# Kernel optimization log

Hardware: AMD Instinct MI355X
Metric: run time of the kernel (lower is better)

The kernel has to match this reference:

```python
import jax, jax.numpy as jnp
import numpy as np

B, N, D, H, I = 16, 1024, 1024, 16, 4096
HS = D // H  # 64
EPS = 1e-5


def setup_inputs() -> dict:
    key = jax.random.key(0)
    ks = jax.random.split(key, 8)
    w = lambda k, shape: (jax.random.normal(k, shape, jnp.float32) * 0.02)
    return {
        'hidden_states': jax.random.normal(ks[0], (B, N, D), jnp.float32),
        'ln1_g': jnp.ones((D,), jnp.float32), 'ln1_b': jnp.zeros((D,), jnp.float32),
        'ln2_g': jnp.ones((D,), jnp.float32), 'ln2_b': jnp.zeros((D,), jnp.float32),
        'wq': w(ks[1], (D, D)), 'bq': jnp.zeros((D,), jnp.float32),
        'wk': w(ks[2], (D, D)), 'bk': jnp.zeros((D,), jnp.float32),
        'wv': w(ks[3], (D, D)), 'bv': jnp.zeros((D,), jnp.float32),
        'w1': w(ks[4], (D, I)), 'b1': jnp.zeros((I,), jnp.float32),
        'w2': w(ks[5], (I, D)), 'b2': jnp.zeros((D,), jnp.float32),
    }


def _layernorm(x, g, b):
    m = jnp.mean(x, axis=-1, keepdims=True)
    v = jnp.var(x, axis=-1, keepdims=True)
    return (x - m) * jax.lax.rsqrt(v + EPS) * g + b


def _split_heads(t):
    # Faithful to transpose_for_scores: reshape (B,N,HS,H) -> (B,H,N,HS)
    # i.e. head h takes the strided feature slice t[..., h::H].
    b, n, _ = t.shape
    return t.reshape(b, n, HS, H).transpose(0, 3, 1, 2)


def _vit_layer(x, ln1_g, ln1_b, ln2_g, ln2_b, wq, bq, wk, bk, wv, bv, w1, b1, w2, b2):
    h = _layernorm(x, ln1_g, ln1_b)
    q = _split_heads(h @ wq + bq)  # [B,H,N,HS]
    k = _split_heads(h @ wk + bk)
    v = _split_heads(h @ wv + bv)
    scores = jax.nn.softmax(jnp.einsum('bhqd,bhkd->bhqk', q, k) / np.sqrt(HS).astype(np.float32), axis=-1)
    attn = jnp.einsum('bhqk,bhkd->bhqd', scores, v)          # [B,H,N,HS]
    attn = attn.transpose(0, 2, 1, 3).reshape(x.shape)       # head-major merge (as in source)
    x = x + attn
    h = _layernorm(x, ln2_g, ln2_b)
    mlp = jax.nn.silu(h @ w1 + b1) @ w2 + b2
    return x + mlp


def reference(hidden_states, ln1_g, ln1_b, ln2_g, ln2_b, wq, bq, wk, bk, wv, bv, w1, b1, w2, b2):
    return _vit_layer(hidden_states, ln1_g, ln1_b, ln2_g, ln2_b, wq, bq, wk, bk, wv, bv, w1, b1, w2, b2)
```

## Files before the change

### kernel.cpp

```cpp
#include <hip/hip_runtime.h>
#include <hip/hip_bf16.h>
#include <stdint.h>

typedef __bf16 bf16;
typedef bf16 bf16x8 __attribute__((ext_vector_type(8)));
typedef bf16 bf16x4 __attribute__((ext_vector_type(4)));
typedef float f32x4 __attribute__((ext_vector_type(4)));

static __device__ __forceinline__ f32x4 mfma16(bf16x8 a, bf16x8 b, f32x4 c) {
    return __builtin_amdgcn_mfma_f32_16x16x32_bf16(a, b, c, 0, 0, 0);
}

static __device__ __forceinline__ void gld16(const bf16* g, bf16* l) {
    __builtin_amdgcn_global_load_lds((const __attribute__((address_space(1))) void*)g,
                                     (__attribute__((address_space(3))) void*)l, 16, 0, 0);
}

static __device__ __forceinline__ uint32_t pkbf(float a, float b) {
    union { bf16 h[2]; uint32_t u; } u_;
    u_.h[0] = (bf16)a; u_.h[1] = (bf16)b;
    return u_.u;
}

static __device__ __forceinline__ void xcd_supertile(int gdx, int gdy,
                                                     int& bx, int& by) {
    const int orig = blockIdx.y * gdx + blockIdx.x;
    const int xcd = orig & 7;
    const int idx = orig >> 3;
    const int CBY = gdy >> 3;
    const int gx = (gdx >= 4) ? 4 : gdx;
    const int gy = (CBY >= 4) ? 4 : CBY;
    const int cells = gx * gy;
    const int st = idx / cells, off = idx % cells;
    const int nstx = gdx / gx;
    const int stx = st % nstx, sty = st / nstx;
    bx = stx * gx + off % gx;
    by = xcd * CBY + sty * gy + off / gx;
}

static __device__ __forceinline__ void tcast_body_p1(
    const float* __restrict__ src, bf16* __restrict__ dst,
    int R, int C, int bx, int by, int tid, float (*t)[33]) {
    const int tx = tid & 31, ty = tid >> 5;
    const int c0 = bx * 32, r0 = by * 32;
#pragma unroll
    for (int j = 0; j < 4; ++j)
        t[ty + j * 8][tx] = src[(size_t)(r0 + ty + j * 8) * C + c0 + tx];
    __syncthreads();
#pragma unroll
    for (int j = 0; j < 4; ++j) {
        const int c = c0 + ty + j * 8;
        const int cp = ((c & 15) << 6) | (c >> 4);
        dst[(size_t)cp * R + r0 + tx] = (bf16)t[tx][ty + j * 8];
    }
}

static __device__ __forceinline__ void tcast_body_p0(
    const float* __restrict__ src, bf16* __restrict__ dst,
    int R, int C, int bx, int by, int tid, float (*t)[33]) {
    const int tx = tid & 31, ty = tid >> 5;
    const int c0 = bx * 32, r0 = by * 32;
#pragma unroll
    for (int j = 0; j < 4; ++j)
        t[ty + j * 8][tx] = src[(size_t)(r0 + ty + j * 8) * C + c0 + tx];
    __syncthreads();
#pragma unroll
    for (int j = 0; j < 4; ++j) {
        const int c = c0 + ty + j * 8;
        dst[(size_t)c * R + r0 + tx] = (bf16)t[tx][ty + j * 8];
    }
}

__global__ __launch_bounds__(256)
void prologue_kernel(const float* __restrict__ wq, const float* __restrict__ wk,
                     const float* __restrict__ wv, const float* __restrict__ w1,
                     const float* __restrict__ w2,
                     const float* __restrict__ bq, const float* __restrict__ bk,
                     const float* __restrict__ bv,
                     const float* __restrict__ x, const float* __restrict__ gg,
                     const float* __restrict__ bb,
                     bf16* __restrict__ Wqkvt, bf16* __restrict__ W1t,
                     bf16* __restrict__ W2t, float* __restrict__ bqkvp,
                     bf16* __restrict__ Xln) {
    __shared__ float t[32][33];
    __shared__ float red[8];
    const int blk = blockIdx.x, tid = threadIdx.x;

    if (blk < 3072) {
        const int seg = blk >> 10, b = blk & 1023;
        const float* src = (seg == 0) ? wq : (seg == 1) ? wk : wv;
        tcast_body_p1(src, Wqkvt + (size_t)seg * 1024 * 1024,
                      1024, 1024, b & 31, b >> 5, tid, t);
    } else if (blk < 7168) {
        const int b = blk - 3072;
        tcast_body_p0(w1, W1t, 1024, 4096, b & 127, b >> 7, tid, t);
    } else if (blk < 11264) {
        const int b = blk - 7168;
        tcast_body_p0(w2, W2t, 4096, 1024, b & 31, b >> 5, tid, t);
    } else if (blk < 11276) {
        const int i = (blk - 11264) * 256 + tid;
        const int seg = i >> 10, c = i & 1023;
        const int src = ((c & 63) << 4) | (c >> 6);
        const float* b = (seg == 0) ? bq : (seg == 1) ? bk : bv;
        bqkvp[i] = b[src];
    } else {
        const int row = blk - 11276;
        const int lane = tid & 63, wid = tid >> 6;
        const float4 v = ((const float4*)(x + (size_t)row * 1024))[tid];
        float s  = v.x + v.y + v.z + v.w;
        float s2 = v.x * v.x + v.y * v.y + v.z * v.z + v.w * v.w;
#pragma unroll
        for (int m = 1; m <= 32; m <<= 1) {
            s  += __shfl_xor(s,  m);
            s2 += __shfl_xor(s2, m);
        }
        if (lane == 0) { red[wid] = s; red[wid + 4] = s2; }
        __syncthreads();
        float ts  = red[0] + red[1] + red[2] + red[3];
        float ts2 = red[4] + red[5] + red[6] + red[7];
        float mean = ts * (1.f / 1024.f);
        float var  = ts2 * (1.f / 1024.f) - mean * mean;
        float rs   = rsqrtf(var + 1e-5f);
        const float4 gv = ((const float4*)gg)[tid];
        const float4 bv4 = ((const float4*)bb)[tid];
        bf16x4 o;
        o[0] = (bf16)((v.x - mean) * rs * gv.x + bv4.x);
        o[1] = (bf16)((v.y - mean) * rs * gv.y + bv4.y);
        o[2] = (bf16)((v.z - mean) * rs * gv.z + bv4.z);
        o[3] = (bf16)((v.w - mean) * rs * gv.w + bv4.w);
        *(bf16x4*)(Xln + (size_t)row * 1024 + tid * 4) = o;
    }
}

__global__ __launch_bounds__(256)
void ln_kernel(const float* __restrict__ x, const float* __restrict__ gg,
               const float* __restrict__ bb, bf16* __restrict__ out) {
    __shared__ float red[8];
    const int row = blockIdx.x, tid = threadIdx.x;
    const int lane = tid & 63, wid = tid >> 6;
    const float4 v = ((const float4*)(x + (size_t)row * 1024))[tid];
    float s  = v.x + v.y + v.z + v.w;
    float s2 = v.x * v.x + v.y * v.y + v.z * v.z + v.w * v.w;
#pragma unroll
    for (int m = 1; m <= 32; m <<= 1) {
        s  += __shfl_xor(s,  m);
        s2 += __shfl_xor(s2, m);
    }
    if (lane == 0) { red[wid] = s; red[wid + 4] = s2; }
    __syncthreads();
    float ts  = red[0] + red[1] + red[2] + red[3];
    float ts2 = red[4] + red[5] + red[6] + red[7];
    float mean = ts * (1.f / 1024.f);
    float var  = ts2 * (1.f / 1024.f) - mean * mean;
    float rs   = rsqrtf(var + 1e-5f);
    const float4 gv = ((const float4*)gg)[tid];
    const float4 bv = ((const float4*)bb)[tid];
    bf16x4 o;
    o[0] = (bf16)((v.x - mean) * rs * gv.x + bv.x);
    o[1] = (bf16)((v.y - mean) * rs * gv.y + bv.y);
    o[2] = (bf16)((v.z - mean) * rs * gv.z + bv.z);
    o[3] = (bf16)((v.w - mean) * rs * gv.w + bv.w);
    *(bf16x4*)(out + (size_t)row * 1024 + tid * 4) = o;
}

template <int MODE>
__global__ __launch_bounds__(256)
void gemm_bt(const bf16* __restrict__ A, const bf16* __restrict__ Bt,
             int M, int N, int K,
             const float* __restrict__ bias_a,
             const float* __restrict__ resid, float* __restrict__ outF,
             bf16* __restrict__ oQ, bf16* __restrict__ oK, bf16* __restrict__ oV,
             bf16* __restrict__ oB) {
    __shared__ alignas(16) bf16 As[3][128 * 32];
    __shared__ alignas(16) bf16 Bs[3][128 * 32];
    const int tid = threadIdx.x;
    const int wid = tid >> 6, lane = tid & 63;
    const int li = lane & 15, g = lane >> 4;

    int bx, by;
    xcd_supertile(gridDim.x, gridDim.y, bx, by);
    const int row0 = by * 128, col0 = bx * 128;

    const int gsrc = ((tid & 3) ^ ((tid >> 3) & 3)) * 8;
    const bf16* gA0 = A + (size_t)(row0 + (tid >> 2)) * K + gsrc;
    const bf16* gA1 = A + (size_t)(row0 + 64 + (tid >> 2)) * K + gsrc;
    const bf16* gB0 = Bt + (size_t)(col0 + (tid >> 2)) * K + gsrc;
    const bf16* gB1 = Bt + (size_t)(col0 + 64 + (tid >> 2)) * K + gsrc;

    const int wr = wid >> 1, wc = wid & 1;
    f32x4 acc[4][4] = {};

    const int nt = K >> 5;
#pragma unroll
    for (int p = 0; p < 2; ++p) {
        const int kk = p << 5;
        gld16(gA0 + kk, &As[p][wid * 512]);
        gld16(gA1 + kk, &As[p][wid * 512 + 2048]);
        gld16(gB0 + kk, &Bs[p][wid * 512]);
        gld16(gB1 + kk, &Bs[p][wid * 512 + 2048]);
    }

    const int sa = (li >> 1) & 3;
    const int rdoff = (g ^ sa) * 8;

    int cur = 0;
    for (int t = 0; t < nt; ++t) {
        if (t + 2 < nt) {
            const int k2 = (t + 2) << 5;
            const int nb = (cur + 2) % 3;
            gld16(gA0 + k2, &As[nb][wid * 512]);
            gld16(gA1 + k2, &As[nb][wid * 512 + 2048]);
            gld16(gB0 + k2, &Bs[nb][wid * 512]);
            gld16(gB1 + k2, &Bs[nb][wid * 512 + 2048]);
            asm volatile("s_waitcnt vmcnt(8)" ::: "memory");
        } else if (t + 1 < nt) {
            asm volatile("s_waitcnt vmcnt(4)" ::: "memory");
        } else {
            asm volatile("s_waitcnt vmcnt(0)" ::: "memory");
        }
        __builtin_amdgcn_s_barrier();
        __builtin_amdgcn_sched_barrier(0);

        bf16x8 af[4], bg[4];
        const bf16* pa = &As[cur][(wr * 64 + li) * 32 + rdoff];
        const bf16* pb = &Bs[cur][(wc * 64 + li) * 32 + rdoff];
#pragma unroll
        for (int i = 0; i < 4; ++i) af[i] = *(const bf16x8*)(pa + i * 512);
#pragma unroll
        for (int j = 0; j < 4; ++j) bg[j] = *(const bf16x8*)(pb + j * 512);
#pragma unroll
        for (int i = 0; i < 4; ++i)
#pragma unroll
            for (int j = 0; j < 4; ++j)
                acc[i][j] = mfma16(af[i], bg[j], acc[i][j]);
        __builtin_amdgcn_sched_barrier(0);
        __builtin_amdgcn_s_barrier();
        cur = (cur + 1) % 3;
    }

    if (MODE == 0) {
        const int seg = col0 >> 10;
        const int h   = ((col0 & 1023) >> 6) + wc;
        const int bb  = row0 >> 10;
        const int n0  = (row0 & 1023) + wr * 64;
        float bias[4];
#pragma unroll
        for (int j = 0; j < 4; ++j) bias[j] = bias_a[col0 + wc * 64 + j * 16 + li];

        if (seg == 2) {
#pragma unroll
            for (int i = 0; i < 4; ++i)
#pragma unroll
                for (int j = 0; j < 4; ++j) {
                    const int d = j * 16 + li;
                    bf16x4 pv;
#pragma unroll
                    for (int r = 0; r < 4; ++r) pv[r] = (bf16)(acc[i][j][r] + bias[j]);
                    *(bf16x4*)(oV + ((size_t)(bb * 16 + h) * 64 + d) * 1024
                                   + n0 + i * 16 + g * 4) = pv;
                }
        } else {
            char* ep = (wid < 3) ? ((char*)&As[0][0] + wid * 8192)
                                 : ((char*)&Bs[0][0]);
            const float scale = (seg == 0) ? 0.125f : 1.0f;
            bf16* og = (seg == 0) ? oQ : oK;
#pragma unroll
            for (int i = 0; i < 4; ++i)
#pragma unroll
                for (int j = 0; j < 4; ++j)
#pragma unroll
                    for (int r = 0; r < 4; ++r) {
                        const int rr = i * 16 + g * 4 + r;
                        const int byte = (rr * 128 + (j * 16 + li) * 2) ^ ((rr & 7) << 4);
                        *(bf16*)(ep + byte) = (bf16)((acc[i][j][r] + bias[j]) * scale);
                    }
            bf16* gb = og + ((size_t)(bb * 16 + h) * 1024 + n0) * 64;
#pragma unroll
            for (int t = 0; t < 8; ++t) {
                const int rr = t * 8 + (lane >> 3);
                const int d0 = (lane & 7) * 8;
                const int byte = (rr * 128 + d0 * 2) ^ ((rr & 7) << 4);
                bf16x8 val = *(const bf16x8*)(ep + byte);
                *(bf16x8*)(gb + (size_t)rr * 64 + d0) = val;
            }
        }
    } else {
#pragma unroll
        for (int i = 0; i < 4; ++i) {
            const int row = row0 + wr * 64 + i * 16 + g * 4;
#pragma unroll
            for (int j = 0; j < 4; ++j) {
                const int col = col0 + wc * 64 + j * 16 + li;
                f32x4 v = acc[i][j];
                if (MODE == 1) {
                    const float bias = bias_a[col];
#pragma unroll
                    for (int r = 0; r < 4; ++r) {
                        float val = v[r] + bias;
                        val = val / (1.f + __expf(-val));
                        oB[(size_t)(row + r) * N + col] = (bf16)val;
                    }
                } else {
                    const float bias = bias_a[col];
#pragma unroll
                    for (int r = 0; r < 4; ++r) {
                        const size_t idx = (size_t)(row + r) * N + col;
                        outF[idx] = v[r] + bias + resid[idx];
                    }
                }
            }
        }
    }
}

template <int MODE>
__global__ __launch_bounds__(512, 2)
void gemm256(const bf16* __restrict__ A, const bf16* __restrict__ Bt,
             int M, int N, int K,
             const float* __restrict__ bias_a,
             const float* __restrict__ resid, float* __restrict__ outF,
             bf16* __restrict__ oB) {
    __shared__ alignas(16) bf16 As[2][256 * 64];
    __shared__ alignas(16) bf16 Bs[2][256 * 64];
    const int tid = threadIdx.x;
    const int wid = tid >> 6, lane = tid & 63;
    const int li = lane & 15, g = lane >> 4;
    const int wm = wid >> 2, wn = wid & 3;

    int bx, by;
    xcd_supertile(gridDim.x, gridDim.y, bx, by);
    const int row0 = by * 256, col0 = bx * 256;

    const int gsrc = ((tid & 7) ^ ((tid >> 3) & 7)) << 3;
    const bf16* gA = A + (size_t)(row0 + (tid >> 3)) * K + gsrc;
    const bf16* gB = Bt + (size_t)(col0 + (tid >> 3)) * K + gsrc;

    f32x4 acc[8][4] = {};
    const int nt = K >> 6;

    const int ro0 = (((0 * 4 + g) ^ (li & 7)) << 3);
    const int ro1 = (((1 * 4 + g) ^ (li & 7)) << 3);

#pragma unroll
    for (int j = 0; j < 4; ++j) {
        gld16(gA + (size_t)(64 * j) * K, &As[0][j * 4096 + (wid << 9)]);
        gld16(gB + (size_t)(64 * j) * K, &Bs[0][j * 4096 + (wid << 9)]);
    }

#define RDA(dst, p)                                                        \
    do {                                                                   \
        _Pragma("unroll")                                                  \
        for (int ii = 0; ii < 2; ++ii) {                                   \
            const int rr = wm * 128 + ((p) * 2 + ii) * 16 + li;            \
            dst[ii][0] = *(const bf16x8*)(At + rr * 64 + ro0);             \
            dst[ii][1] = *(const bf16x8*)(At + rr * 64 + ro1);             \
        }                                                                  \
    } while (0)

#define MFMAP(p, src)                                                      \
    do {                                                                   \
        __builtin_amdgcn_s_setprio(1);                                     \
        _Pragma("unroll")                                                  \
        for (int ii = 0; ii < 2; ++ii)                                     \
            _Pragma("unroll")                                              \
            for (int jf = 0; jf < 4; ++jf) {                               \
                acc[(p) * 2 + ii][jf] = mfma16(src[ii][0], bfr[jf][0],     \
                                               acc[(p) * 2 + ii][jf]);     \
                acc[(p) * 2 + ii][jf] = mfma16(src[ii][1], bfr[jf][1],     \
                                               acc[(p) * 2 + ii][jf]);     \
            }                                                              \
        __builtin_amdgcn_s_setprio(0);                                     \
    } while (0)

    for (int t = 0; t < nt; ++t) {
        asm volatile("s_waitcnt vmcnt(0)" ::: "memory");
        __builtin_amdgcn_s_barrier();
        __builtin_amdgcn_sched_barrier(0);

        const bf16* At = &As[t & 1][0];
        const bf16* Bl = &Bs[t & 1][0];
        bf16* Asn = &As[(t & 1) ^ 1][0];
        bf16* Bsn = &Bs[(t & 1) ^ 1][0];
        const bool pf = (t + 1 < nt);
        const size_t koff = (size_t)(t + 1) << 6;

        bf16x8 bfr[4][2];
#pragma unroll
        for (int jf = 0; jf < 4; ++jf) {
            const int rb = wn * 64 + jf * 16 + li;
            bfr[jf][0] = *(const bf16x8*)(Bl + rb * 64 + ro0);
            bfr[jf][1] = *(const bf16x8*)(Bl + rb * 64 + ro1);
        }
        bf16x8 afA[2][2], afB[2][2];
        RDA(afA, 0);
        if (pf) {
            gld16(gB + koff,                   Bsn + (wid << 9));
            gld16(gB + (size_t)64 * K + koff,  Bsn + 4096 + (wid << 9));
            gld16(gB + (size_t)128 * K + koff, Bsn + 2 * 4096 + (wid << 9));
            gld16(gB + (size_t)192 * K + koff, Bsn + 3 * 4096 + (wid << 9));
        }
        RDA(afB, 1);
        asm volatile("s_waitcnt lgkmcnt(4)" ::: "memory");
        __builtin_amdgcn_sched_barrier(0);
        MFMAP(0, afA);

        RDA(afA, 2);
        asm volatile("s_waitcnt lgkmcnt(4)" ::: "memory");
        __builtin_amdgcn_sched_barrier(0);
        MFMAP(1, afB);

        if (pf) {
            gld16(gA + koff,                   Asn + (wid << 9));
            gld16(gA + (size_t)64 * K + koff,  Asn + 4096 + (wid << 9));
            gld16(gA + (size_t)128 * K + koff, Asn + 2 * 4096 + (wid << 9));
            gld16(gA + (size_t)192 * K + koff, Asn + 3 * 4096 + (wid << 9));
        }
        RDA(afB, 3);
        asm volatile("s_waitcnt lgkmcnt(4)" ::: "memory");
        __builtin_amdgcn_sched_barrier(0);
        MFMAP(2, afA);

        asm volatile("s_waitcnt lgkmcnt(0)" ::: "memory");
        __builtin_amdgcn_sched_barrier(0);
        MFMAP(3, afB);
    }
#undef RDA
#undef MFMAP

#pragma unroll
    for (int i = 0; i < 8; ++i) {
        const int row = row0 + wm * 128 + i * 16 + g * 4;
#pragma unroll
        for (int jf = 0; jf < 4; ++jf) {
            const int col = col0 + wn * 64 + jf * 16 + li;
            const float bias = bias_a[col];
            if (MODE == 1) {
#pragma unroll
                for (int r = 0; r < 4; ++r) {
                    float val = acc[i][jf][r] + bias;
                    val = val / (1.f + __expf(-val));
                    oB[(size_t)(row + r) * N + col] = (bf16)val;
                }
            } else {
#pragma unroll
                for (int r = 0; r < 4; ++r) {
                    const size_t idx = (size_t)(row + r) * N + col;
                    outF[idx] = acc[i][jf][r] + bias + resid[idx];
                }
            }
        }
    }
}

__global__ __launch_bounds__(256)
void attn_kernel(const bf16* __restrict__ Q, const bf16* __restrict__ Kb,
                 const bf16* __restrict__ Vt, const float* __restrict__ x,
                 float* __restrict__ out) {
    __shared__ alignas(16) bf16 Kl[2][4096];
    __shared__ alignas(16) bf16 Vl[2][4096];
    __shared__ alignas(16) char Ps[4][4096];
    const int tid = threadIdx.x, wid = tid >> 6, lane = tid & 63;
    const int li = lane & 15, g = lane >> 4;
    const int bid = blockIdx.x;
    const int bh = (bid & 7) + ((bid >> 6) << 3);
    const int qt = (bid >> 3) & 7;
    const int b = bh >> 4, h = bh & 15;
    const size_t base = (size_t)bh << 16;
    const bf16* Qp = Q + base + (size_t)(qt * 128 + wid * 32) * 64;
    const bf16* Kp = Kb + base;
    const bf16* Vp = Vt + base;
    char* psw = Ps[wid];
    const int swz = (li & 7) << 4;

    const int srow = lane >> 3;
    const int sslot = (lane & 7) ^ srow;

    bf16x8 aq[2][2];
#pragma unroll
    for (int fr = 0; fr < 2; ++fr)
#pragma unroll
        for (int ks = 0; ks < 2; ++ks)
            aq[fr][ks] = *(const bf16x8*)(Qp + (fr * 16 + li) * 64 + ks * 32 + g * 8);

#pragma unroll
    for (int hh = 0; hh < 2; ++hh) {
        const int r = wid * 16 + hh * 8 + srow;
        gld16(Kp + (size_t)r * 64 + sslot * 8, &Kl[0][(wid * 16 + hh * 8) * 64]);
        gld16(Vp + (size_t)r * 1024 + sslot * 8, &Vl[0][(wid * 16 + hh * 8) * 64]);
    }
    asm volatile("s_waitcnt vmcnt(0)" ::: "memory");
    __builtin_amdgcn_s_barrier();

    f32x4 o[2][4] = {};
    float mrun[2] = {-1e30f, -1e30f}, lrun[2] = {0.f, 0.f};

    for (int kt = 0; kt < 16; ++kt) {
        const int cur = kt & 1;
        const bf16* Kt = Kl[cur];
        const bf16* Vtl = Vl[cur];
        if (kt < 15) {
            const int nb = (kt + 1) * 64;
#pragma unroll
            for (int hh = 0; hh < 2; ++hh) {
                const int r = wid * 16 + hh * 8 + srow;
                gld16(Kp + (size_t)(nb + r) * 64 + sslot * 8,
                      &Kl[cur ^ 1][(wid * 16 + hh * 8) * 64]);
                gld16(Vp + (size_t)r * 1024 + nb + sslot * 8,
                      &Vl[cur ^ 1][(wid * 16 + hh * 8) * 64]);
            }
            asm volatile("s_waitcnt vmcnt(4)" ::: "memory");
        } else {
            asm volatile("s_waitcnt vmcnt(0)" ::: "memory");
        }
        __builtin_amdgcn_s_barrier();
        __builtin_amdgcn_sched_barrier(0);

        f32x4 s[2][4] = {};
        __builtin_amdgcn_s_setprio(1);
#pragma unroll
        for (int jc = 0; jc < 4; ++jc) {
            const int row = jc * 16 + li;
#pragma unroll
            for (int ks = 0; ks < 2; ++ks) {
                bf16x8 kf = *(const bf16x8*)(Kt + row * 64 + (((ks * 4 + g) ^ (li & 7)) * 8));
                s[0][jc] = mfma16(kf, aq[0][ks], s[0][jc]);
                s[1][jc] = mfma16(kf, aq[1][ks], s[1][jc]);
            }
        }
        __builtin_amdgcn_s_setprio(0);

#pragma unroll
        for (int fr = 0; fr < 2; ++fr) {
            float mj[4];
#pragma unroll
            for (int jc = 0; jc < 4; ++jc)
                mj[jc] = fmaxf(fmaxf(s[fr][jc][0], s[fr][jc][1]),
                               fmaxf(s[fr][jc][2], s[fr][jc][3]));
            float mx = fmaxf(fmaxf(mj[0], mj[1]), fmaxf(mj[2], mj[3]));
            mx = fmaxf(mx, __shfl_xor(mx, 16));
            mx = fmaxf(mx, __shfl_xor(mx, 32));
            if (!__all(mx <= mrun[fr] + 8.f)) {
                const float mnew = fmaxf(mrun[fr], mx);
                const float alpha = __expf(mrun[fr] - mnew);
                mrun[fr] = mnew;
                lrun[fr] *= alpha;
#pragma unroll
                for (int jd = 0; jd < 4; ++jd) o[fr][jd] *= alpha;
            }
            float pj[4];
#pragma unroll
            for (int jc = 0; jc < 4; ++jc) {
#pragma unroll
                for (int r = 0; r < 4; ++r)
                    s[fr][jc][r] = __expf(s[fr][jc][r] - mrun[fr]);
                pj[jc] = (s[fr][jc][0] + s[fr][jc][1]) + (s[fr][jc][2] + s[fr][jc][3]);
            }
            float ps = (pj[0] + pj[1]) + (pj[2] + pj[3]);
            ps += __shfl_xor(ps, 16);
            ps += __shfl_xor(ps, 32);
            lrun[fr] += ps;

            const int qb = (fr * 16 + li) * 128;
#pragma unroll
            for (int jc = 0; jc < 4; ++jc) {
                uint2 w;
                w.x = pkbf(s[fr][jc][0], s[fr][jc][1]);
                w.y = pkbf(s[fr][jc][2], s[fr][jc][3]);
                *(uint2*)(psw + ((qb + jc * 32 + g * 8) ^ swz)) = w;
            }
        }

#pragma unroll
        for (int ks2 = 0; ks2 < 2; ++ks2) {
            bf16x8 pa0 = *(const bf16x8*)(psw + ((li * 128 + ks2 * 64 + g * 16) ^ swz));
            bf16x8 pa1 = *(const bf16x8*)(psw + (((16 + li) * 128 + ks2 * 64 + g * 16) ^ swz));
            __builtin_amdgcn_s_setprio(1);
#pragma unroll
            for (int jd = 0; jd < 4; ++jd) {
                const int row = jd * 16 + li;
                bf16x8 vf = *(const bf16x8*)(Vtl + row * 64 + (((ks2 * 4 + g) ^ (li & 7)) * 8));
                o[0][jd] = mfma16(vf, pa0, o[0][jd]);
                o[1][jd] = mfma16(vf, pa1, o[1][jd]);
            }
            __builtin_amdgcn_s_setprio(0);
        }
        __builtin_amdgcn_sched_barrier(0);
        __builtin_amdgcn_s_barrier();
    }

    const int n0 = qt * 128 + wid * 32;
#pragma unroll
    for (int fr = 0; fr < 2; ++fr) {
        const float inv = 1.f / lrun[fr];
        const int n = n0 + fr * 16 + li;
        const size_t rowb = (size_t)(b * 1024 + n) * 1024 + h * 64;
#pragma unroll
        for (int jd = 0; jd < 4; ++jd) {
            const int c = jd * 16 + g * 4;
            const float4 xv = *(const float4*)(x + rowb + c);
            float4 ov;
            ov.x = xv.x + o[fr][jd][0] * inv;
            ov.y = xv.y + o[fr][jd][1] * inv;
            ov.z = xv.z + o[fr][jd][2] * inv;
            ov.w = xv.w + o[fr][jd][3] * inv;
            *(float4*)(out + rowb + c) = ov;
        }
    }
}

extern "C" void kernel_launch(void* const* d_in, const int* in_sizes, int n_in,
                              void* d_out, int out_size, void* d_ws, size_t ws_size,
                              hipStream_t stream) {
    const float* x    = (const float*)d_in[0];
    const float* ln1g = (const float*)d_in[1];
    const float* ln1b = (const float*)d_in[2];
    const float* ln2g = (const float*)d_in[3];
    const float* ln2b = (const float*)d_in[4];
    const float* wq   = (const float*)d_in[5];
    const float* bq   = (const float*)d_in[6];
    const float* wk   = (const float*)d_in[7];
    const float* bk   = (const float*)d_in[8];
    const float* wv   = (const float*)d_in[9];
    const float* bv   = (const float*)d_in[10];
    const float* w1   = (const float*)d_in[11];
    const float* b1   = (const float*)d_in[12];
    const float* w2   = (const float*)d_in[13];
    const float* b2   = (const float*)d_in[14];

    char* ws = (char*)d_ws;
    const size_t MB = 1024 * 1024;
    bf16*  Wqkvt = (bf16*)(ws);
    bf16*  W1t   = (bf16*)(ws + 6 * MB);
    bf16*  W2t   = (bf16*)(ws + 14 * MB);
    float* ares  = (float*)(ws + 22 * MB);
    bf16*  Xln   = (bf16*)(ws + 86 * MB);
    bf16*  Qb    = (bf16*)(ws + 118 * MB);
    bf16*  Kbuf  = (bf16*)(ws + 150 * MB);
    bf16*  Vtb   = (bf16*)(ws + 182 * MB);
    bf16*  mid   = (bf16*)(ws + 118 * MB);
    float* bqkvp = (float*)(ws + 245 * MB);

    prologue_kernel<<<27660, 256, 0, stream>>>(wq, wk, wv, w1, w2,
        bq, bk, bv, x, ln1g, ln1b, Wqkvt, W1t, W2t, bqkvp, Xln);

    gemm_bt<0><<<dim3(24, 128), 256, 0, stream>>>(Xln, Wqkvt, 16384, 3072, 1024,
        bqkvp, nullptr, nullptr, Qb, Kbuf, Vtb, nullptr);

    attn_kernel<<<2048, 256, 0, stream>>>(Qb, Kbuf, Vtb, x, ares);

    ln_kernel<<<16384, 256, 0, stream>>>(ares, ln2g, ln2b, Xln);

    gemm256<1><<<dim3(16, 64), 512, 0, stream>>>(Xln, W1t, 16384, 4096, 1024,
        b1, nullptr, nullptr, mid);

    gemm256<2><<<dim3(4, 64), 512, 0, stream>>>(mid, W2t, 16384, 1024, 4096,
        b2, ares, (float*)d_out, nullptr);
}
```

Measured before the change: 644.0 us.

## Store attention residual in bf16 and use exp2-based softmax

The post-attention residual buffer is now written as bf16 instead of fp32. It is then read back as bf16 by the second layernorm and by the final GEMM's residual add, which halves traffic for that 64MB intermediate. Softmax moves to exp2f by folding log2(e) into the Q scale, with the rescale threshold adjusted to match. The cost is reduced precision in the residual path that feeds the output.

```diff
diff --git a/kernel.cpp b/kernel.cpp
--- a/kernel.cpp
+++ b/kernel.cpp
@@ -133,14 +133,16 @@
 }
 
 __global__ __launch_bounds__(256)
-void ln_kernel(const float* __restrict__ x, const float* __restrict__ gg,
-               const float* __restrict__ bb, bf16* __restrict__ out) {
+void ln_bf_kernel(const bf16* __restrict__ x, const float* __restrict__ gg,
+                  const float* __restrict__ bb, bf16* __restrict__ out) {
     __shared__ float red[8];
     const int row = blockIdx.x, tid = threadIdx.x;
     const int lane = tid & 63, wid = tid >> 6;
-    const float4 v = ((const float4*)(x + (size_t)row * 1024))[tid];
-    float s  = v.x + v.y + v.z + v.w;
-    float s2 = v.x * v.x + v.y * v.y + v.z * v.z + v.w * v.w;
+    const bf16x4 vb = *(const bf16x4*)(x + (size_t)row * 1024 + tid * 4);
+    const float v0 = (float)vb[0], v1 = (float)vb[1];
+    const float v2 = (float)vb[2], v3 = (float)vb[3];
+    float s  = v0 + v1 + v2 + v3;
+    float s2 = v0 * v0 + v1 * v1 + v2 * v2 + v3 * v3;
 #pragma unroll
     for (int m = 1; m <= 32; m <<= 1) {
         s  += __shfl_xor(s,  m);
@@ -156,10 +158,10 @@
     const float4 gv = ((const float4*)gg)[tid];
     const float4 bv = ((const float4*)bb)[tid];
     bf16x4 o;
-    o[0] = (bf16)((v.x - mean) * rs * gv.x + bv.x);
-    o[1] = (bf16)((v.y - mean) * rs * gv.y + bv.y);
-    o[2] = (bf16)((v.z - mean) * rs * gv.z + bv.z);
-    o[3] = (bf16)((v.w - mean) * rs * gv.w + bv.w);
+    o[0] = (bf16)((v0 - mean) * rs * gv.x + bv.x);
+    o[1] = (bf16)((v1 - mean) * rs * gv.y + bv.y);
+    o[2] = (bf16)((v2 - mean) * rs * gv.z + bv.z);
+    o[3] = (bf16)((v3 - mean) * rs * gv.w + bv.w);
     *(bf16x4*)(out + (size_t)row * 1024 + tid * 4) = o;
 }
 
@@ -262,7 +264,7 @@
         } else {
             char* ep = (wid < 3) ? ((char*)&As[0][0] + wid * 8192)
                                  : ((char*)&Bs[0][0]);
-            const float scale = (seg == 0) ? 0.125f : 1.0f;
+            const float scale = (seg == 0) ? 0.18033688f : 1.0f;
             bf16* og = (seg == 0) ? oQ : oK;
 #pragma unroll
             for (int i = 0; i < 4; ++i)
@@ -318,7 +320,7 @@
 void gemm256(const bf16* __restrict__ A, const bf16* __restrict__ Bt,
              int M, int N, int K,
              const float* __restrict__ bias_a,
-             const float* __restrict__ resid, float* __restrict__ outF,
+             const bf16* __restrict__ resid, float* __restrict__ outF,
              bf16* __restrict__ oB) {
     __shared__ alignas(16) bf16 As[2][256 * 64];
     __shared__ alignas(16) bf16 Bs[2][256 * 64];
@@ -445,7 +447,7 @@
 #pragma unroll
                 for (int r = 0; r < 4; ++r) {
                     const size_t idx = (size_t)(row + r) * N + col;
-                    outF[idx] = acc[i][jf][r] + bias + resid[idx];
+                    outF[idx] = acc[i][jf][r] + bias + (float)resid[idx];
                 }
             }
         }
@@ -455,7 +457,7 @@
 __global__ __launch_bounds__(256)
 void attn_kernel(const bf16* __restrict__ Q, const bf16* __restrict__ Kb,
                  const bf16* __restrict__ Vt, const float* __restrict__ x,
-                 float* __restrict__ out) {
+                 bf16* __restrict__ out) {
     __shared__ alignas(16) bf16 Kl[2][4096];
     __shared__ alignas(16) bf16 Vl[2][4096];
     __shared__ alignas(16) char Ps[4][4096];
@@ -539,9 +541,9 @@
             float mx = fmaxf(fmaxf(mj[0], mj[1]), fmaxf(mj[2], mj[3]));
             mx = fmaxf(mx, __shfl_xor(mx, 16));
             mx = fmaxf(mx, __shfl_xor(mx, 32));
-            if (!__all(mx <= mrun[fr] + 8.f)) {
+            if (!__all(mx <= mrun[fr] + 11.5416f)) {
                 const float mnew = fmaxf(mrun[fr], mx);
-                const float alpha = __expf(mrun[fr] - mnew);
+                const float alpha = exp2f(mrun[fr] - mnew);
                 mrun[fr] = mnew;
                 lrun[fr] *= alpha;
 #pragma unroll
@@ -552,7 +554,7 @@
             for (int jc = 0; jc < 4; ++jc) {
 #pragma unroll
                 for (int r = 0; r < 4; ++r)
-                    s[fr][jc][r] = __expf(s[fr][jc][r] - mrun[fr]);
+                    s[fr][jc][r] = exp2f(s[fr][jc][r] - mrun[fr]);
                 pj[jc] = (s[fr][jc][0] + s[fr][jc][1]) + (s[fr][jc][2] + s[fr][jc][3]);
             }
             float ps = (pj[0] + pj[1]) + (pj[2] + pj[3]);
@@ -598,12 +600,12 @@
         for (int jd = 0; jd < 4; ++jd) {
             const int c = jd * 16 + g * 4;
             const float4 xv = *(const float4*)(x + rowb + c);
-            float4 ov;
-            ov.x = xv.x + o[fr][jd][0] * inv;
-            ov.y = xv.y + o[fr][jd][1] * inv;
-            ov.z = xv.z + o[fr][jd][2] * inv;
-            ov.w = xv.w + o[fr][jd][3] * inv;
-            *(float4*)(out + rowb + c) = ov;
+            bf16x4 ov;
+            ov[0] = (bf16)(xv.x + o[fr][jd][0] * inv);
+            ov[1] = (bf16)(xv.y + o[fr][jd][1] * inv);
+            ov[2] = (bf16)(xv.z + o[fr][jd][2] * inv);
+            ov[3] = (bf16)(xv.w + o[fr][jd][3] * inv);
+            *(bf16x4*)(out + rowb + c) = ov;
         }
     }
 }
@@ -629,16 +631,16 @@
 
     char* ws = (char*)d_ws;
     const size_t MB = 1024 * 1024;
-    bf16*  Wqkvt = (bf16*)(ws);
-    bf16*  W1t   = (bf16*)(ws + 6 * MB);
-    bf16*  W2t   = (bf16*)(ws + 14 * MB);
-    float* ares  = (float*)(ws + 22 * MB);
-    bf16*  Xln   = (bf16*)(ws + 86 * MB);
-    bf16*  Qb    = (bf16*)(ws + 118 * MB);
-    bf16*  Kbuf  = (bf16*)(ws + 150 * MB);
-    bf16*  Vtb   = (bf16*)(ws + 182 * MB);
-    bf16*  mid   = (bf16*)(ws + 118 * MB);
-    float* bqkvp = (float*)(ws + 245 * MB);
+    bf16*  Wqkvt  = (bf16*)(ws);
+    bf16*  W1t    = (bf16*)(ws + 6 * MB);
+    bf16*  W2t    = (bf16*)(ws + 14 * MB);
+    bf16*  aresb  = (bf16*)(ws + 22 * MB);
+    bf16*  Xln    = (bf16*)(ws + 86 * MB);
+    bf16*  Qb     = (bf16*)(ws + 118 * MB);
+    bf16*  Kbuf   = (bf16*)(ws + 150 * MB);
+    bf16*  Vtb    = (bf16*)(ws + 182 * MB);
+    bf16*  mid    = (bf16*)(ws + 118 * MB);
+    float* bqkvp  = (float*)(ws + 245 * MB);
 
     prologue_kernel<<<27660, 256, 0, stream>>>(wq, wk, wv, w1, w2,
         bq, bk, bv, x, ln1g, ln1b, Wqkvt, W1t, W2t, bqkvp, Xln);
@@ -646,13 +648,13 @@
     gemm_bt<0><<<dim3(24, 128), 256, 0, stream>>>(Xln, Wqkvt, 16384, 3072, 1024,
         bqkvp, nullptr, nullptr, Qb, Kbuf, Vtb, nullptr);
 
-    attn_kernel<<<2048, 256, 0, stream>>>(Qb, Kbuf, Vtb, x, ares);
-
-    ln_kernel<<<16384, 256, 0, stream>>>(ares, ln2g, ln2b, Xln);
+    attn_kernel<<<2048, 256, 0, stream>>>(Qb, Kbuf, Vtb, x, aresb);
+
+    ln_bf_kernel<<<16384, 256, 0, stream>>>(aresb, ln2g, ln2b, Xln);
 
     gemm256<1><<<dim3(16, 64), 512, 0, stream>>>(Xln, W1t, 16384, 4096, 1024,
         b1, nullptr, nullptr, mid);
 
     gemm256<2><<<dim3(4, 64), 512, 0, stream>>>(mid, W2t, 16384, 1024, 4096,
-        b2, ares, (float*)d_out, nullptr);
-}
+        b2, aresb, (float*)d_out, nullptr);
+}
```

New measurement: 646.9 us. No clear change (+0.5%).
